# Optimization experiments

Measured on AMD Instinct MI355X. Metric: run time of the kernel, lower is better.

## Reference

```python
import jax, jax.numpy as jnp
import numpy as np

NEG_SLOPE = 0.2  # PyG GATConv default negative_slope
EPS = 1e-16


def gat_conv(x, src, dst, num_nodes, W, att_src, att_dst, bias, concat):
    """PyG-style GATConv (eval mode, no dropout). att_*: [H, C]."""
    H, C = att_src.shape
    h = (x @ W).reshape(num_nodes, H, C)                      # [N,H,C]
    a_s = jnp.einsum('nhc,hc->nh', h, att_src)                # [N,H]
    a_d = jnp.einsum('nhc,hc->nh', h, att_dst)                # [N,H]
    e = jax.nn.leaky_relu(a_s[src] + a_d[dst], NEG_SLOPE)     # [E,H]
    # segment softmax over edges grouped by destination node
    m = jax.lax.stop_gradient(jax.ops.segment_max(e, dst, num_segments=num_nodes))
    ex = jnp.exp(e - m[dst])
    denom = jax.ops.segment_sum(ex, dst, num_segments=num_nodes)
    alpha = ex / (denom[dst] + EPS)                           # [E,H]
    msg = h[src] * alpha[:, :, None]                          # [E,H,C]
    out = jax.ops.segment_sum(msg, dst, num_segments=num_nodes)  # [N,H,C]
    out = out.reshape(num_nodes, H * C) if concat else out.mean(axis=1)
    return out + bias


def setup_inputs() -> dict:
    key = jax.random.key(0)
    ks = jax.random.split(key, 12)
    N, E = 65536, 1310720
    IN, HID, OUT, HEADS = 768, 128, 2, 8
    C1 = HID // HEADS  # 16
    s = 0.05
    return {
        'x': jax.random.normal(ks[0], (N, IN), jnp.float32),
        'edge_index': jax.random.randint(ks[1], (2, E), 0, N, jnp.int64),
        'W1': jax.random.normal(ks[2], (IN, HEADS * C1), jnp.float32) * s,
        'att_src1': jax.random.normal(ks[3], (HEADS, C1), jnp.float32) * s,
        'att_dst1': jax.random.normal(ks[4], (HEADS, C1), jnp.float32) * s,
        'b1': jnp.zeros((HID,), jnp.float32),
        'Wp': jax.random.normal(ks[5], (IN, HID), jnp.float32) * s,
        'bp': jnp.zeros((HID,), jnp.float32),
        'W2': jax.random.normal(ks[6], (HID, OUT), jnp.float32) * s,
        'att_src2': jax.random.normal(ks[7], (1, OUT), jnp.float32) * s,
        'att_dst2': jax.random.normal(ks[8], (1, OUT), jnp.float32) * s,
        'b2': jnp.zeros((OUT,), jnp.float32),
    }


def reference(x, edge_index, W1, att_src1, att_dst1, b1, Wp, bp, W2, att_src2, att_dst2, b2):
    N = x.shape[0]
    loops = jnp.arange(N, dtype=edge_index.dtype)  # add_self_loops=True
    src = jnp.concatenate([edge_index[0], loops])
    dst = jnp.concatenate([edge_index[1], loops])
    # eval mode: dropout is identity
    h1 = gat_conv(x, src, dst, N, W1, att_src1, att_dst1, b1, concat=True)
    h = jax.nn.elu(h1 + x @ Wp + bp)  # residual projection + ELU
    return gat_conv(h, src, dst, N, W2, att_src2, att_dst2, b2, concat=False)
```

## Files before the change

kernel.cpp:

```cpp
#include <hip/hip_runtime.h>
#include <hip/hip_bf16.h>
#include <math.h>

#define NEG_SLOPE 0.2f

typedef __attribute__((ext_vector_type(8))) short short8;
typedef __attribute__((ext_vector_type(4))) float float4v;

__device__ __forceinline__ unsigned f2bf(float f) {
  unsigned u = __builtin_bit_cast(unsigned, f);
  return (u + 0x7fffu + ((u >> 16) & 1u)) >> 16;
}
__device__ __forceinline__ float bflo(unsigned u) {
  return __builtin_bit_cast(float, u << 16);
}
__device__ __forceinline__ float bfhi(unsigned u) {
  return __builtin_bit_cast(float, u & 0xffff0000u);
}

__global__ __launch_bounds__(256) void convert_w(const float* __restrict__ W1,
                                                 const float* __restrict__ Wp,
                                                 short* __restrict__ Wt) {
  int k = blockIdx.x;
  int c = threadIdx.x;
  float v = (c < 128) ? W1[k * 128 + c] : Wp[k * 128 + (c - 128)];
  Wt[(size_t)c * 768 + k] = (short)f2bf(v);
}

__global__ __launch_bounds__(256) void gemm_mfma(const float* __restrict__ x,
                                                 const short* __restrict__ Wt,
                                                 float* __restrict__ proj,
                                                 unsigned* __restrict__ h1bf) {
  __shared__ short As[64][40];
  __shared__ short Bs[256][40];
  const int tid = threadIdx.x;
  const int wave = tid >> 6, lane = tid & 63;
  const int l15 = lane & 15, l4 = lane >> 4;
  const int row0 = blockIdx.x * 64;

  const int ar = tid >> 3;
  const int ak = (tid & 7) * 4;
  const int bc = tid >> 2;
  const int bk = (tid & 3) * 8;

  float4v acc[4][4] = {};

  for (int k0 = 0; k0 < 768; k0 += 32) {
#pragma unroll
    for (int i = 0; i < 2; i++) {
      int r = i * 32 + ar;
      float4 f = *(const float4*)&x[(size_t)(row0 + r) * 768 + k0 + ak];
      uint2 p;
      p.x = f2bf(f.x) | (f2bf(f.y) << 16);
      p.y = f2bf(f.z) | (f2bf(f.w) << 16);
      *(uint2*)&As[r][ak] = p;
    }
#pragma unroll
    for (int i = 0; i < 4; i++) {
      int c = i * 64 + bc;
      uint4 v = *(const uint4*)&Wt[(size_t)c * 768 + k0 + bk];
      *(uint4*)&Bs[c][bk] = v;
    }
    __syncthreads();

    short8 afr[4];
#pragma unroll
    for (int rt = 0; rt < 4; rt++)
      afr[rt] = *(const short8*)&As[rt * 16 + l15][l4 * 8];
#pragma unroll
    for (int ct = 0; ct < 4; ct++) {
      short8 bfr = *(const short8*)&Bs[wave * 64 + ct * 16 + l15][l4 * 8];
#pragma unroll
      for (int rt = 0; rt < 4; rt++)
        acc[rt][ct] =
            __builtin_amdgcn_mfma_f32_16x16x32_bf16(afr[rt], bfr, acc[rt][ct], 0, 0, 0);
    }
    __syncthreads();
  }

  const int colbase = wave * 64;
  if (wave < 2) {
#pragma unroll
    for (int ct = 0; ct < 4; ct++) {
      const int c = colbase + ct * 16 + l15;
#pragma unroll
      for (int rt = 0; rt < 4; rt++) {
#pragma unroll
        for (int r = 0; r < 4; r++) {
          const int R = row0 + rt * 16 + l4 * 4 + r;
          unsigned u = f2bf(acc[rt][ct][r]);
          unsigned up = __shfl_xor(u, 1);
          if ((l15 & 1) == 0) h1bf[(size_t)R * 64 + (c >> 1)] = u | (up << 16);
        }
      }
    }
  } else {
#pragma unroll
    for (int ct = 0; ct < 4; ct++) {
      const int c = colbase - 128 + ct * 16 + l15;
#pragma unroll
      for (int rt = 0; rt < 4; rt++) {
#pragma unroll
        for (int r = 0; r < 4; r++) {
          const int R = row0 + rt * 16 + l4 * 4 + r;
          proj[(size_t)R * 128 + c] = acc[rt][ct][r];
        }
      }
    }
  }
}

__global__ __launch_bounds__(256) void attn1b(const uint4* __restrict__ h1bf4,
                                              const float* __restrict__ att_src1,
                                              const float* __restrict__ att_dst1,
                                              float* __restrict__ a_s1,
                                              float* __restrict__ a_d1) {
  const int t = blockIdx.x * 256 + threadIdx.x;
  const int n = t >> 3, h = t & 7;
  uint4 q0 = h1bf4[(size_t)n * 16 + h * 2];
  uint4 q1 = h1bf4[(size_t)n * 16 + h * 2 + 1];
  float v[16];
  v[0] = bflo(q0.x); v[1] = bfhi(q0.x); v[2] = bflo(q0.y); v[3] = bfhi(q0.y);
  v[4] = bflo(q0.z); v[5] = bfhi(q0.z); v[6] = bflo(q0.w); v[7] = bfhi(q0.w);
  v[8] = bflo(q1.x); v[9] = bfhi(q1.x); v[10] = bflo(q1.y); v[11] = bfhi(q1.y);
  v[12] = bflo(q1.z); v[13] = bfhi(q1.z); v[14] = bflo(q1.w); v[15] = bfhi(q1.w);
  float as = 0.f, ad = 0.f;
#pragma unroll
  for (int i = 0; i < 16; i++) {
    as += v[i] * att_src1[h * 16 + i];
    ad += v[i] * att_dst1[h * 16 + i];
  }
  a_s1[t] = as;
  a_d1[t] = ad;
}

__global__ void init_counts(int* counts, int N) {
  int i = blockIdx.x * blockDim.x + threadIdx.x;
  if (i < N) counts[i] = 1;
}

__global__ void hist_kernel(const int* __restrict__ dst, int* counts, int E) {
  int i = blockIdx.x * blockDim.x + threadIdx.x;
  int base = i * 4;
  if (base + 3 < E) {
    int4 d = *(const int4*)&dst[base];
    atomicAdd(&counts[d.x], 1);
    atomicAdd(&counts[d.y], 1);
    atomicAdd(&counts[d.z], 1);
    atomicAdd(&counts[d.w], 1);
  } else {
    for (int j = base; j < E; j++) atomicAdd(&counts[dst[j]], 1);
  }
}

__global__ __launch_bounds__(256) void scan_a(const int* __restrict__ counts,
                                              int* offsets, int* bsum) {
  __shared__ int s[256];
  int t = threadIdx.x, idx = blockIdx.x * 256 + t;
  int v = counts[idx];
  s[t] = v;
  __syncthreads();
  for (int d = 1; d < 256; d <<= 1) {
    int x = (t >= d) ? s[t - d] : 0;
    __syncthreads();
    s[t] += x;
    __syncthreads();
  }
  offsets[idx] = s[t] - v;
  if (t == 255) bsum[blockIdx.x] = s[t];
}

__global__ __launch_bounds__(256) void scan_b(int* bsum) {
  __shared__ int s[256];
  int t = threadIdx.x;
  int v = bsum[t];
  s[t] = v;
  __syncthreads();
  for (int d = 1; d < 256; d <<= 1) {
    int x = (t >= d) ? s[t - d] : 0;
    __syncthreads();
    s[t] += x;
    __syncthreads();
  }
  bsum[t] = s[t] - v;
}

__global__ __launch_bounds__(256) void scan_c(int* offsets, const int* bsum,
                                              int* cursor, int* sortedsrc,
                                              int N, int Etot) {
  int t = threadIdx.x, idx = blockIdx.x * 256 + t;
  int off = offsets[idx] + bsum[blockIdx.x];
  offsets[idx] = off;
  sortedsrc[off] = idx;
  cursor[idx] = off + 1;
  if (idx == 0) offsets[N] = Etot;
}

__global__ void scatter_edges(const int* __restrict__ src,
                              const int* __restrict__ dst, int* cursor,
                              int* sortedsrc, int E) {
  int i = blockIdx.x * blockDim.x + threadIdx.x;
  int base = i * 4;
  if (base + 3 < E) {
    int4 s = *(const int4*)&src[base];
    int4 d = *(const int4*)&dst[base];
    sortedsrc[atomicAdd(&cursor[d.x], 1)] = s.x;
    sortedsrc[atomicAdd(&cursor[d.y], 1)] = s.y;
    sortedsrc[atomicAdd(&cursor[d.z], 1)] = s.z;
    sortedsrc[atomicAdd(&cursor[d.w], 1)] = s.w;
  } else {
    for (int j = base; j < E; j++)
      sortedsrc[atomicAdd(&cursor[dst[j]], 1)] = src[j];
  }
}

__global__ __launch_bounds__(256) void agg1_fused(
    const uint4* __restrict__ h1bf4, const float* __restrict__ proj,
    const float* __restrict__ a_s1, const float* __restrict__ a_d1,
    const int* __restrict__ offsets, const int* __restrict__ sortedsrc,
    const float* __restrict__ b1, const float* __restrict__ bp,
    const float* __restrict__ W2, const float* __restrict__ att_s2,
    const float* __restrict__ att_d2, float* __restrict__ h2,
    float* __restrict__ as2, float* __restrict__ ad2) {
  const int t = threadIdx.x;
  const int n = blockIdx.x * 16 + (t >> 4);
  const int k = t & 15;
  const int hd = k >> 1;
  const float ad = a_d1[n * 8 + hd];
  const int begin = offsets[n], end = offsets[n + 1];
  float acc[8] = {};
  float aw = 0.f;
  int j = begin;
  for (; j + 4 <= end; j += 4) {
    int s0 = sortedsrc[j], s1 = sortedsrc[j + 1];
    int s2 = sortedsrc[j + 2], s3 = sortedsrc[j + 3];
    float e0 = a_s1[s0 * 8 + hd], e1 = a_s1[s1 * 8 + hd];
    float e2 = a_s1[s2 * 8 + hd], e3 = a_s1[s3 * 8 + hd];
    uint4 q0 = h1bf4[(size_t)s0 * 16 + k];
    uint4 q1 = h1bf4[(size_t)s1 * 16 + k];
    uint4 q2 = h1bf4[(size_t)s2 * 16 + k];
    uint4 q3 = h1bf4[(size_t)s3 * 16 + k];
    e0 += ad; e1 += ad; e2 += ad; e3 += ad;
    float w0 = __expf(e0 > 0.f ? e0 : NEG_SLOPE * e0);
    float w1 = __expf(e1 > 0.f ? e1 : NEG_SLOPE * e1);
    float w2 = __expf(e2 > 0.f ? e2 : NEG_SLOPE * e2);
    float w3 = __expf(e3 > 0.f ? e3 : NEG_SLOPE * e3);
    acc[0] += w0 * bflo(q0.x) + w1 * bflo(q1.x) + w2 * bflo(q2.x) + w3 * bflo(q3.x);
    acc[1] += w0 * bfhi(q0.x) + w1 * bfhi(q1.x) + w2 * bfhi(q2.x) + w3 * bfhi(q3.x);
    acc[2] += w0 * bflo(q0.y) + w1 * bflo(q1.y) + w2 * bflo(q2.y) + w3 * bflo(q3.y);
    acc[3] += w0 * bfhi(q0.y) + w1 * bfhi(q1.y) + w2 * bfhi(q2.y) + w3 * bfhi(q3.y);
    acc[4] += w0 * bflo(q0.z) + w1 * bflo(q1.z) + w2 * bflo(q2.z) + w3 * bflo(q3.z);
    acc[5] += w0 * bfhi(q0.z) + w1 * bfhi(q1.z) + w2 * bfhi(q2.z) + w3 * bfhi(q3.z);
    acc[6] += w0 * bflo(q0.w) + w1 * bflo(q1.w) + w2 * bflo(q2.w) + w3 * bflo(q3.w);
    acc[7] += w0 * bfhi(q0.w) + w1 * bfhi(q1.w) + w2 * bfhi(q2.w) + w3 * bfhi(q3.w);
    aw += (w0 + w1) + (w2 + w3);
  }
  for (; j < end; j++) {
    int s0 = sortedsrc[j];
    float e0 = a_s1[s0 * 8 + hd] + ad;
    uint4 q0 = h1bf4[(size_t)s0 * 16 + k];
    float w0 = __expf(e0 > 0.f ? e0 : NEG_SLOPE * e0);
    acc[0] += w0 * bflo(q0.x);
    acc[1] += w0 * bfhi(q0.x);
    acc[2] += w0 * bflo(q0.y);
    acc[3] += w0 * bfhi(q0.y);
    acc[4] += w0 * bflo(q0.z);
    acc[5] += w0 * bfhi(q0.z);
    acc[6] += w0 * bflo(q0.w);
    acc[7] += w0 * bfhi(q0.w);
    aw += w0;
  }
  const float inv = 1.f / (aw + 1e-16f);
  const float4 pj0 = *(const float4*)&proj[(size_t)n * 128 + k * 8];
  const float4 pj1 = *(const float4*)&proj[(size_t)n * 128 + k * 8 + 4];
  const float4 b1a = *(const float4*)&b1[k * 8];
  const float4 b1b = *(const float4*)&b1[k * 8 + 4];
  const float4 bpa = *(const float4*)&bp[k * 8];
  const float4 bpb = *(const float4*)&bp[k * 8 + 4];
  float v[8];
  v[0] = acc[0] * inv + pj0.x + b1a.x + bpa.x;
  v[1] = acc[1] * inv + pj0.y + b1a.y + bpa.y;
  v[2] = acc[2] * inv + pj0.z + b1a.z + bpa.z;
  v[3] = acc[3] * inv + pj0.w + b1a.w + bpa.w;
  v[4] = acc[4] * inv + pj1.x + b1b.x + bpb.x;
  v[5] = acc[5] * inv + pj1.y + b1b.y + bpb.y;
  v[6] = acc[6] * inv + pj1.z + b1b.z + bpb.z;
  v[7] = acc[7] * inv + pj1.w + b1b.w + bpb.w;
  float p0 = 0.f, p1 = 0.f;
#pragma unroll
  for (int i = 0; i < 8; i++) {
    float vi = v[i] > 0.f ? v[i] : (__expf(v[i]) - 1.f);
    float2 w2 = *(const float2*)&W2[(k * 8 + i) * 2];
    p0 += vi * w2.x;
    p1 += vi * w2.y;
  }
#pragma unroll
  for (int off = 8; off; off >>= 1) {
    p0 += __shfl_xor(p0, off);
    p1 += __shfl_xor(p1, off);
  }
  if (k == 0) {
    h2[2 * n] = p0;
    h2[2 * n + 1] = p1;
    as2[n] = p0 * att_s2[0] + p1 * att_s2[1];
    ad2[n] = p0 * att_d2[0] + p1 * att_d2[1];
  }
}

__global__ __launch_bounds__(256) void agg2(
    const float* __restrict__ h2, const float* __restrict__ as2,
    const float* __restrict__ ad2, const int* __restrict__ offsets,
    const int* __restrict__ sortedsrc, const float* __restrict__ b2,
    float* __restrict__ out, int N) {
  const int node = blockIdx.x * 16 + (threadIdx.x >> 4);
  const int lane = threadIdx.x & 15;
  const int begin = offsets[node], end = offsets[node + 1];
  const float ad = ad2[node];
  float acc0 = 0.f, acc1 = 0.f, aw = 0.f;
  for (int j = begin + lane; j < end; j += 16) {
    int s = sortedsrc[j];
    float e = as2[s] + ad;
    float w = __expf(e > 0.f ? e : NEG_SLOPE * e);
    float2 hh = *(const float2*)&h2[2 * s];
    acc0 += w * hh.x;
    acc1 += w * hh.y;
    aw += w;
  }
#pragma unroll
  for (int off = 8; off; off >>= 1) {
    acc0 += __shfl_xor(acc0, off);
    acc1 += __shfl_xor(acc1, off);
    aw += __shfl_xor(aw, off);
  }
  if (lane == 0) {
    float inv = 1.f / (aw + 1e-16f);
    out[2 * node] = acc0 * inv + b2[0];
    out[2 * node + 1] = acc1 * inv + b2[1];
  }
}

extern "C" void kernel_launch(void* const* d_in, const int* in_sizes, int n_in,
                              void* d_out, int out_size, void* d_ws,
                              size_t ws_size, hipStream_t stream) {
  const float* x = (const float*)d_in[0];
  const int* edge_index = (const int*)d_in[1];
  const float* W1 = (const float*)d_in[2];
  const float* att_src1 = (const float*)d_in[3];
  const float* att_dst1 = (const float*)d_in[4];
  const float* b1 = (const float*)d_in[5];
  const float* Wp = (const float*)d_in[6];
  const float* bp = (const float*)d_in[7];
  const float* W2 = (const float*)d_in[8];
  const float* att_src2 = (const float*)d_in[9];
  const float* att_dst2 = (const float*)d_in[10];
  const float* b2 = (const float*)d_in[11];
  float* out = (float*)d_out;

  const int N = in_sizes[0] / 768;
  const int E = in_sizes[1] / 2;
  const int Etot = E + N;
  const int* src = edge_index;
  const int* dst = edge_index + E;

  char* ws = (char*)d_ws;
  size_t off = 0;
  auto alloc = [&](size_t bytes) {
    size_t cur = off;
    off += (bytes + 255) & ~(size_t)255;
    return (void*)(ws + cur);
  };
  float* proj = (float*)alloc((size_t)N * 128 * 4);
  unsigned* h1bf = (unsigned*)alloc((size_t)N * 64 * 4);
  float* a_s1 = (float*)alloc((size_t)N * 8 * 4);
  float* a_d1 = (float*)alloc((size_t)N * 8 * 4);
  float* h2 = (float*)alloc((size_t)N * 2 * 4);
  float* as2 = (float*)alloc((size_t)N * 4);
  float* ad2 = (float*)alloc((size_t)N * 4);
  int* counts = (int*)alloc((size_t)N * 4);
  int* offsets = (int*)alloc(((size_t)N + 1) * 4);
  int* cursor = (int*)alloc((size_t)N * 4);
  int* bsum = (int*)alloc(256 * 4);
  int* sortedsrc = (int*)alloc((size_t)Etot * 4);
  short* Wt = (short*)alloc((size_t)256 * 768 * 2);

  convert_w<<<768, 256, 0, stream>>>(W1, Wp, Wt);
  gemm_mfma<<<N / 64, 256, 0, stream>>>(x, Wt, proj, h1bf);
  attn1b<<<N * 8 / 256, 256, 0, stream>>>((const uint4*)h1bf, att_src1,
                                          att_dst1, a_s1, a_d1);
  init_counts<<<(N + 255) / 256, 256, 0, stream>>>(counts, N);
  hist_kernel<<<(E / 4 + 255) / 256, 256, 0, stream>>>(dst, counts, E);
  scan_a<<<N / 256, 256, 0, stream>>>(counts, offsets, bsum);
  scan_b<<<1, 256, 0, stream>>>(bsum);
  scan_c<<<N / 256, 256, 0, stream>>>(offsets, bsum, cursor, sortedsrc, N,
                                      Etot);
  scatter_edges<<<(E / 4 + 255) / 256, 256, 0, stream>>>(src, dst, cursor,
                                                         sortedsrc, E);
  agg1_fused<<<N / 16, 256, 0, stream>>>((const uint4*)h1bf, proj, a_s1, a_d1,
                                         offsets, sortedsrc, b1, bp, W2,
                                         att_src2, att_dst2, h2, as2, ad2);
  agg2<<<N / 16, 256, 0, stream>>>(h2, as2, ad2, offsets, sortedsrc, b2, out,
                                   N);
}
```

Measured before the change: 573.5 us.

## Prefetch GEMM tiles into registers and derive edge ranks from histogram atomics

```diff
diff --git a/kernel.cpp b/kernel.cpp
--- a/kernel.cpp
+++ b/kernel.cpp
@@ -16,6 +16,11 @@
 }
 __device__ __forceinline__ float bfhi(unsigned u) {
   return __builtin_bit_cast(float, u & 0xffff0000u);
+}
+__device__ __forceinline__ unsigned cvtpk(float lo, float hi) {
+  unsigned r;
+  asm("v_cvt_pk_bf16_f32 %0, %1, %2" : "=v"(r) : "v"(lo), "v"(hi));
+  return r;
 }
 
 __global__ __launch_bounds__(256) void convert_w(const float* __restrict__ W1,
@@ -43,26 +48,43 @@
   const int bc = tid >> 2;
   const int bk = (tid & 3) * 8;
 
+  const float* xp0 = &x[(size_t)(row0 + ar) * 768 + ak];
+  const float* xp1 = &x[(size_t)(row0 + 32 + ar) * 768 + ak];
+  const short* wp = &Wt[(size_t)bc * 768 + bk];
+
   float4v acc[4][4] = {};
 
-  for (int k0 = 0; k0 < 768; k0 += 32) {
-#pragma unroll
-    for (int i = 0; i < 2; i++) {
-      int r = i * 32 + ar;
-      float4 f = *(const float4*)&x[(size_t)(row0 + r) * 768 + k0 + ak];
-      uint2 p;
-      p.x = f2bf(f.x) | (f2bf(f.y) << 16);
-      p.y = f2bf(f.z) | (f2bf(f.w) << 16);
-      *(uint2*)&As[r][ak] = p;
+  float4 a0 = *(const float4*)xp0;
+  float4 a1 = *(const float4*)xp1;
+  uint4 w0 = *(const uint4*)(wp);
+  uint4 w1 = *(const uint4*)(wp + 49152);
+  uint4 w2 = *(const uint4*)(wp + 98304);
+  uint4 w3 = *(const uint4*)(wp + 147456);
+  {
+    uint2 p;
+    p.x = cvtpk(a0.x, a0.y);
+    p.y = cvtpk(a0.z, a0.w);
+    *(uint2*)&As[ar][ak] = p;
+    p.x = cvtpk(a1.x, a1.y);
+    p.y = cvtpk(a1.z, a1.w);
+    *(uint2*)&As[32 + ar][ak] = p;
+    *(uint4*)&Bs[bc][bk] = w0;
+    *(uint4*)&Bs[64 + bc][bk] = w1;
+    *(uint4*)&Bs[128 + bc][bk] = w2;
+    *(uint4*)&Bs[192 + bc][bk] = w3;
+  }
+
+  for (int t = 0; t < 24; t++) {
+    __syncthreads();
+    const int kn = (t + 1) * 32;
+    if (t < 23) {
+      a0 = *(const float4*)(xp0 + kn);
+      a1 = *(const float4*)(xp1 + kn);
+      w0 = *(const uint4*)(wp + kn);
+      w1 = *(const uint4*)(wp + 49152 + kn);
+      w2 = *(const uint4*)(wp + 98304 + kn);
+      w3 = *(const uint4*)(wp + 147456 + kn);
     }
-#pragma unroll
-    for (int i = 0; i < 4; i++) {
-      int c = i * 64 + bc;
-      uint4 v = *(const uint4*)&Wt[(size_t)c * 768 + k0 + bk];
-      *(uint4*)&Bs[c][bk] = v;
-    }
-    __syncthreads();
-
     short8 afr[4];
 #pragma unroll
     for (int rt = 0; rt < 4; rt++)
@@ -76,6 +98,19 @@
             __builtin_amdgcn_mfma_f32_16x16x32_bf16(afr[rt], bfr, acc[rt][ct], 0, 0, 0);
     }
     __syncthreads();
+    if (t < 23) {
+      uint2 p;
+      p.x = cvtpk(a0.x, a0.y);
+      p.y = cvtpk(a0.z, a0.w);
+      *(uint2*)&As[ar][ak] = p;
+      p.x = cvtpk(a1.x, a1.y);
+      p.y = cvtpk(a1.z, a1.w);
+      *(uint2*)&As[32 + ar][ak] = p;
+      *(uint4*)&Bs[bc][bk] = w0;
+      *(uint4*)&Bs[64 + bc][bk] = w1;
+      *(uint4*)&Bs[128 + bc][bk] = w2;
+      *(uint4*)&Bs[192 + bc][bk] = w3;
+    }
   }
 
   const int colbase = wave * 64;
@@ -139,17 +174,20 @@
   if (i < N) counts[i] = 1;
 }
 
-__global__ void hist_kernel(const int* __restrict__ dst, int* counts, int E) {
+__global__ void hist_kernel(const int* __restrict__ dst, int* counts,
+                            int* __restrict__ rank, int E) {
   int i = blockIdx.x * blockDim.x + threadIdx.x;
   int base = i * 4;
   if (base + 3 < E) {
     int4 d = *(const int4*)&dst[base];
-    atomicAdd(&counts[d.x], 1);
-    atomicAdd(&counts[d.y], 1);
-    atomicAdd(&counts[d.z], 1);
-    atomicAdd(&counts[d.w], 1);
+    int4 r;
+    r.x = atomicAdd(&counts[d.x], 1);
+    r.y = atomicAdd(&counts[d.y], 1);
+    r.z = atomicAdd(&counts[d.z], 1);
+    r.w = atomicAdd(&counts[d.w], 1);
+    *(int4*)&rank[base] = r;
   } else {
-    for (int j = base; j < E; j++) atomicAdd(&counts[dst[j]], 1);
+    for (int j = base; j < E; j++) rank[j] = atomicAdd(&counts[dst[j]], 1);
   }
 }
 
@@ -186,31 +224,32 @@
 }
 
 __global__ __launch_bounds__(256) void scan_c(int* offsets, const int* bsum,
-                                              int* cursor, int* sortedsrc,
-                                              int N, int Etot) {
+                                              int* sortedsrc, int N, int Etot) {
   int t = threadIdx.x, idx = blockIdx.x * 256 + t;
   int off = offsets[idx] + bsum[blockIdx.x];
   offsets[idx] = off;
   sortedsrc[off] = idx;
-  cursor[idx] = off + 1;
   if (idx == 0) offsets[N] = Etot;
 }
 
 __global__ void scatter_edges(const int* __restrict__ src,
-                              const int* __restrict__ dst, int* cursor,
-                              int* sortedsrc, int E) {
+                              const int* __restrict__ dst,
+                              const int* __restrict__ rank,
+                              const int* __restrict__ offsets,
+                              int* __restrict__ sortedsrc, int E) {
   int i = blockIdx.x * blockDim.x + threadIdx.x;
   int base = i * 4;
   if (base + 3 < E) {
     int4 s = *(const int4*)&src[base];
     int4 d = *(const int4*)&dst[base];
-    sortedsrc[atomicAdd(&cursor[d.x], 1)] = s.x;
-    sortedsrc[atomicAdd(&cursor[d.y], 1)] = s.y;
-    sortedsrc[atomicAdd(&cursor[d.z], 1)] = s.z;
-    sortedsrc[atomicAdd(&cursor[d.w], 1)] = s.w;
+    int4 r = *(const int4*)&rank[base];
+    sortedsrc[offsets[d.x] + r.x] = s.x;
+    sortedsrc[offsets[d.y] + r.y] = s.y;
+    sortedsrc[offsets[d.z] + r.z] = s.z;
+    sortedsrc[offsets[d.w] + r.w] = s.w;
   } else {
     for (int j = base; j < E; j++)
-      sortedsrc[atomicAdd(&cursor[dst[j]], 1)] = src[j];
+      sortedsrc[offsets[dst[j]] + rank[j]] = src[j];
   }
 }
 
@@ -378,7 +417,7 @@
   float* ad2 = (float*)alloc((size_t)N * 4);
   int* counts = (int*)alloc((size_t)N * 4);
   int* offsets = (int*)alloc(((size_t)N + 1) * 4);
-  int* cursor = (int*)alloc((size_t)N * 4);
+  int* rank = (int*)alloc((size_t)E * 4);
   int* bsum = (int*)alloc(256 * 4);
   int* sortedsrc = (int*)alloc((size_t)Etot * 4);
   short* Wt = (short*)alloc((size_t)256 * 768 * 2);
@@ -388,13 +427,12 @@
   attn1b<<<N * 8 / 256, 256, 0, stream>>>((const uint4*)h1bf, att_src1,
                                           att_dst1, a_s1, a_d1);
   init_counts<<<(N + 255) / 256, 256, 0, stream>>>(counts, N);
-  hist_kernel<<<(E / 4 + 255) / 256, 256, 0, stream>>>(dst, counts, E);
+  hist_kernel<<<(E / 4 + 255) / 256, 256, 0, stream>>>(dst, counts, rank, E);
   scan_a<<<N / 256, 256, 0, stream>>>(counts, offsets, bsum);
   scan_b<<<1, 256, 0, stream>>>(bsum);
-  scan_c<<<N / 256, 256, 0, stream>>>(offsets, bsum, cursor, sortedsrc, N,
-                                      Etot);
-  scatter_edges<<<(E / 4 + 255) / 256, 256, 0, stream>>>(src, dst, cursor,
-                                                         sortedsrc, E);
+  scan_c<<<N / 256, 256, 0, stream>>>(offsets, bsum, sortedsrc, N, Etot);
+  scatter_edges<<<(E / 4 + 255) / 256, 256, 0, stream>>>(src, dst, rank,
+                                                         offsets, sortedsrc, E);
   agg1_fused<<<N / 16, 256, 0, stream>>>((const uint4*)h1bf, proj, a_s1, a_d1,
                                          offsets, sortedsrc, b1, bp, W2,
                                          att_src2, att_dst2, h2, as2, ad2);
```

Measured after the change: 525.7 us. 1.09x faster.
